# Performance work log

Measured on AMD Instinct MI355X. Metric: run time of the kernel, lower is better.

## Reference

```python
import jax, jax.numpy as jnp
import numpy as np
import math

CHUNK = 64

def _linear(x, W, b):
    # torch nn.Linear: y = x @ W.T + b
    return jnp.einsum('bsd,ed->bse', x, W) + b

def setup_inputs() -> dict:
    key = jax.random.key(0)
    ks = jax.random.split(key, 10)
    B, S, D = 4, 4096, 512
    scale = 0.02
    inp = {
        'x': jax.random.normal(ks[0], (B, S, D), jnp.float32),
        'base_phases': jax.random.normal(ks[1], (S, D), jnp.float32) * math.pi,
        'Wk': jax.random.normal(ks[2], (D, D), jnp.float32) * scale,
        'bk': jnp.zeros((D,), jnp.float32),
        'Wv': jax.random.normal(ks[3], (D, D), jnp.float32) * scale,
        'bv': jnp.zeros((D,), jnp.float32),
        'Wq': jax.random.normal(ks[4], (D, D), jnp.float32) * scale,
        'bq': jnp.zeros((D,), jnp.float32),
        'Wkm': jax.random.normal(ks[5], (D, D), jnp.float32) * scale,
        'bkm': jnp.zeros((D,), jnp.float32),
        'Wqm': jax.random.normal(ks[6], (D, D), jnp.float32) * scale,
        'bqm': jnp.zeros((D,), jnp.float32),
        'mod_scale': jnp.ones((1,), jnp.float32) * 0.1,
        'ln_g': jnp.ones((D,), jnp.float32),
        'ln_b': jnp.zeros((D,), jnp.float32),
        'Wo': jax.random.normal(ks[7], (D, D), jnp.float32) * scale,
        'bo': jnp.zeros((D,), jnp.float32),
    }
    return inp

def reference(x, base_phases, Wk, bk, Wv, bv, Wq, bq, Wkm, bkm, Wqm, bqm, mod_scale, ln_g, ln_b, Wo, bo):
    B, S, D = x.shape
    bp = base_phases[:S][None]                      # [1,S,D]
    key = _linear(x, Wk, bk)
    value = _linear(x, Wv, bv)
    query = _linear(x, Wq, bq)
    key_phase = bp + _linear(key, Wkm, bkm) * mod_scale
    query_phase = bp + _linear(query, Wqm, bqm) * mod_scale
    bound_real = value * jnp.cos(key_phase)
    bound_imag = value * jnp.sin(key_phase)
    # chunked cumulative memory (S divisible by CHUNK -> no padding)
    nC = S // CHUNK
    br = bound_real.reshape(B, nC, CHUNK, D)
    bi = bound_imag.reshape(B, nC, CHUNK, D)
    qp = query_phase.reshape(B, nC, CHUNK, D)
    mem_real = jnp.cumsum(br, axis=2)
    mem_imag = jnp.cumsum(bi, axis=2)
    retrieved = (mem_real * jnp.cos(qp) + mem_imag * jnp.sin(qp)).reshape(B, S, D)
    retrieved = retrieved / math.sqrt(D)
    # LayerNorm + Linear (to_out)
    mu = jnp.mean(retrieved, axis=-1, keepdims=True)
    var = jnp.mean((retrieved - mu) ** 2, axis=-1, keepdims=True)
    normed = (retrieved - mu) / jnp.sqrt(var + 1e-5) * ln_g + ln_b
    out = _linear(normed, Wo, bo)
    return x + out
```

## Files before the change

### kernel.cpp

```cpp
#include <hip/hip_runtime.h>
#include <hip/hip_bf16.h>


typedef __attribute__((ext_vector_type(8))) short short8;
typedef __attribute__((ext_vector_type(4))) float f32x4;

#define M_TOK   16384
#define DIM     512
#define NCHUNK  64

__device__ __forceinline__ void gll16(const void* g, void* l) {
  __builtin_amdgcn_global_load_lds(
      (const __attribute__((address_space(1))) unsigned int*)g,
      (__attribute__((address_space(3))) unsigned int*)l, 16, 0, 0);
}

__device__ __forceinline__ uint2 pack4bf(float4 v) {
  union { __hip_bfloat16 h[4]; uint2 u; } t;
  t.h[0] = __float2bfloat16(v.x);
  t.h[1] = __float2bfloat16(v.y);
  t.h[2] = __float2bfloat16(v.z);
  t.h[3] = __float2bfloat16(v.w);
  return t.u;
}

__global__ __launch_bounds__(256) void cvt_f32_bf16(
    const float* __restrict__ s, __hip_bfloat16* __restrict__ d, int n4) {
  int i = blockIdx.x * 256 + threadIdx.x;
  if (i >= n4) return;
  ((uint2*)d)[i] = pack4bf(((const float4*)s)[i]);
}

__global__ __launch_bounds__(256) void prep(
    const float* __restrict__ Wv, const float* __restrict__ Wo,
    const float* __restrict__ bv,
    const float* __restrict__ Wkm, const float* __restrict__ Wqm,
    const float* __restrict__ Wk, const float* __restrict__ Wq,
    const float* __restrict__ bk, const float* __restrict__ bkm,
    const float* __restrict__ bq, const float* __restrict__ bqm,
    __hip_bfloat16* __restrict__ Wall, float* __restrict__ bc1,
    __hip_bfloat16* __restrict__ Wm_bf, __hip_bfloat16* __restrict__ WT_bf) {
  const int b = blockIdx.x;
  const int tid = threadIdx.x;
  if (b < 512) {
    int m = b >> 8;
    int idx = ((b & 255) * 256 + tid) * 4;
    const float* src = m ? Wo : Wv;
    __hip_bfloat16* dst = Wall + (m ? (size_t)1536 * 512 : 0);
    ((uint2*)dst)[idx >> 2] = pack4bf(*(const float4*)(src + idx));
    int t = b * 256 + tid;
    if (t < 512) bc1[t] = bv[t];
  } else if (b < 1024) {
    int bb = b - 512;
    int m = bb >> 8;
    int idx = ((bb & 255) * 256 + tid) * 4;
    const float* src = m ? Wqm : Wkm;
    ((uint2*)(Wm_bf + (size_t)m * 262144))[idx >> 2] =
        pack4bf(*(const float4*)(src + idx));
  } else if (b < 1152) {
    __shared__ float tile[64][65];
    int bb = b - 1024;
    int z = bb >> 6;
    int tl = bb & 63;
    int tr = tl >> 3, tc = tl & 7;
    const float* src = z ? Wq : Wk;
#pragma unroll
    for (int i = 0; i < 4; i++) {
      int r = (tid >> 4) + 16 * i;
      int c4 = (tid & 15) * 4;
      float4 v = *(const float4*)(src + (size_t)(tr * 64 + r) * 512 +
                                  tc * 64 + c4);
      tile[r][c4 + 0] = v.x;
      tile[r][c4 + 1] = v.y;
      tile[r][c4 + 2] = v.z;
      tile[r][c4 + 3] = v.w;
    }
    __syncthreads();
    int orow = tid >> 2;
    int seg = tid & 3;
    __hip_bfloat16* dst = WT_bf + (size_t)z * 262144 +
                          (size_t)(tc * 64 + orow) * 512 + tr * 64 + seg * 16;
#pragma unroll
    for (int q = 0; q < 4; q++) {
      float4 v;
      v.x = tile[seg * 16 + q * 4 + 0][orow];
      v.y = tile[seg * 16 + q * 4 + 1][orow];
      v.z = tile[seg * 16 + q * 4 + 2][orow];
      v.w = tile[seg * 16 + q * 4 + 3][orow];
      *(uint2*)(dst + q * 4) = pack4bf(v);
    }
  } else {
    int row = (b - 1152) * 4 + (tid >> 6);
    int lane = tid & 63;
    int z = row >> 9;
    int i = row & 511;
    const float* Wm = z ? Wqm : Wkm;
    const float* b0 = z ? bq : bk;
    const float* bm = z ? bqm : bkm;
    const float4* w4 = (const float4*)(Wm + (size_t)i * 512 + lane * 8);
    const float4* v4 = (const float4*)(b0 + lane * 8);
    float4 w0 = w4[0], w1 = w4[1], c0 = v4[0], c1 = v4[1];
    float acc = w0.x * c0.x + w0.y * c0.y + w0.z * c0.z + w0.w * c0.w +
                w1.x * c1.x + w1.y * c1.y + w1.z * c1.z + w1.w * c1.w;
#pragma unroll
    for (int off = 32; off; off >>= 1) acc += __shfl_xor(acc, off, 64);
    if (lane == 0) bc1[512 + z * 512 + i] = acc + bm[i];
  }
}

template <int EPI>
__global__ __launch_bounds__(256) void gemm_bt(
    const __hip_bfloat16* __restrict__ A, int lda,
    const __hip_bfloat16* __restrict__ Bt,
    const float* __restrict__ bias,
    void* __restrict__ Cout, int ldc,
    const float* __restrict__ resid) {
  constexpr int K = 512, BK = 32;
  __shared__ __align__(16) __hip_bfloat16 As[128 * BK];
  __shared__ __align__(16) __hip_bfloat16 Bs[128 * BK];

  const int tid  = threadIdx.x;
  const int lane = tid & 63;
  const int w    = tid >> 6;
  const int wm   = w >> 1;
  const int wn   = w & 1;
  const int m0   = blockIdx.y * 128;
  const int n0   = blockIdx.x * 128;

  const int rS0    = (w * 2 + 0) * 16 + (lane >> 2);
  const int rS1    = (w * 2 + 1) * 16 + (lane >> 2);
  const int kInRow = (lane & 3) * 8;
  const __hip_bfloat16* gA0 = A + (size_t)(m0 + rS0) * lda + kInRow;
  const __hip_bfloat16* gA1 = A + (size_t)(m0 + rS1) * lda + kInRow;
  const __hip_bfloat16* gB0 = Bt + (size_t)(n0 + rS0) * K + kInRow;
  const __hip_bfloat16* gB1 = Bt + (size_t)(n0 + rS1) * K + kInRow;
  char* ldsA0 = (char*)As + (w * 2 + 0) * 1024;
  char* ldsA1 = (char*)As + (w * 2 + 1) * 1024;
  char* ldsB0 = (char*)Bs + (w * 2 + 0) * 1024;
  char* ldsB1 = (char*)Bs + (w * 2 + 1) * 1024;

  f32x4 acc[4][4] = {};

  const int rfA = lane & 15;
  const int rfK = (lane >> 4) * 8;

  for (int kt = 0; kt < K; kt += BK) {
    __syncthreads();
    gll16(gA0 + kt, ldsA0);
    gll16(gA1 + kt, ldsA1);
    gll16(gB0 + kt, ldsB0);
    gll16(gB1 + kt, ldsB1);
    __syncthreads();

    short8 af[4], bf[4];
#pragma unroll
    for (int i = 0; i < 4; i++)
      af[i] = *(const short8*)(As + (wm * 64 + i * 16 + rfA) * BK + rfK);
#pragma unroll
    for (int j = 0; j < 4; j++)
      bf[j] = *(const short8*)(Bs + (wn * 64 + j * 16 + rfA) * BK + rfK);
#pragma unroll
    for (int i = 0; i < 4; i++)
#pragma unroll
      for (int j = 0; j < 4; j++)
        acc[i][j] = __builtin_amdgcn_mfma_f32_16x16x32_bf16(
            af[i], bf[j], acc[i][j], 0, 0, 0);
  }

  const int cq = lane >> 4;
#pragma unroll
  for (int i = 0; i < 4; i++) {
    int row = m0 + wm * 64 + i * 16 + cq * 4;
#pragma unroll
    for (int j = 0; j < 4; j++) {
      int col = n0 + wn * 64 + j * 16 + (lane & 15);
      float bz = bias[col];
#pragma unroll
      for (int r = 0; r < 4; r++) {
        float v = acc[i][j][r] + bz;
        size_t o = (size_t)(row + r) * ldc + col;
        if (EPI == 0) {
          ((__hip_bfloat16*)Cout)[o] = __float2bfloat16(v);
        } else {
          ((float*)Cout)[o] = v + resid[o];
        }
      }
    }
  }
}

__global__ __launch_bounds__(256) void gemm_compose(
    const __hip_bfloat16* __restrict__ Wm_bf,
    const __hip_bfloat16* __restrict__ WT_bf,
    __hip_bfloat16* __restrict__ Wall) {
  constexpr int K = 512, BK = 32;
  const __hip_bfloat16* A  = Wm_bf + (size_t)blockIdx.z * 262144;
  const __hip_bfloat16* Bt = WT_bf + (size_t)blockIdx.z * 262144;
  __hip_bfloat16* C = Wall + (size_t)(512 + blockIdx.z * 512) * 512;
  __shared__ __align__(16) __hip_bfloat16 As[128 * BK];
  __shared__ __align__(16) __hip_bfloat16 Bs[128 * BK];

  const int tid  = threadIdx.x;
  const int lane = tid & 63;
  const int w    = tid >> 6;
  const int wm   = w >> 1;
  const int wn   = w & 1;
  const int m0   = blockIdx.y * 128;
  const int n0   = blockIdx.x * 128;

  const int rS0    = (w * 2 + 0) * 16 + (lane >> 2);
  const int rS1    = (w * 2 + 1) * 16 + (lane >> 2);
  const int kInRow = (lane & 3) * 8;
  const __hip_bfloat16* gA0 = A + (size_t)(m0 + rS0) * K + kInRow;
  const __hip_bfloat16* gA1 = A + (size_t)(m0 + rS1) * K + kInRow;
  const __hip_bfloat16* gB0 = Bt + (size_t)(n0 + rS0) * K + kInRow;
  const __hip_bfloat16* gB1 = Bt + (size_t)(n0 + rS1) * K + kInRow;
  char* ldsA0 = (char*)As + (w * 2 + 0) * 1024;
  char* ldsA1 = (char*)As + (w * 2 + 1) * 1024;
  char* ldsB0 = (char*)Bs + (w * 2 + 0) * 1024;
  char* ldsB1 = (char*)Bs + (w * 2 + 1) * 1024;

  f32x4 acc[4][4] = {};
  const int rfA = lane & 15;
  const int rfK = (lane >> 4) * 8;

  for (int kt = 0; kt < K; kt += BK) {
    __syncthreads();
    gll16(gA0 + kt, ldsA0);
    gll16(gA1 + kt, ldsA1);
    gll16(gB0 + kt, ldsB0);
    gll16(gB1 + kt, ldsB1);
    __syncthreads();

    short8 af[4], bf[4];
#pragma unroll
    for (int i = 0; i < 4; i++)
      af[i] = *(const short8*)(As + (wm * 64 + i * 16 + rfA) * BK + rfK);
#pragma unroll
    for (int j = 0; j < 4; j++)
      bf[j] = *(const short8*)(Bs + (wn * 64 + j * 16 + rfA) * BK + rfK);
#pragma unroll
    for (int i = 0; i < 4; i++)
#pragma unroll
      for (int j = 0; j < 4; j++)
        acc[i][j] = __builtin_amdgcn_mfma_f32_16x16x32_bf16(
            af[i], bf[j], acc[i][j], 0, 0, 0);
  }

  const int cq = lane >> 4;
#pragma unroll
  for (int i = 0; i < 4; i++) {
    int row = m0 + wm * 64 + i * 16 + cq * 4;
#pragma unroll
    for (int j = 0; j < 4; j++) {
      int col = n0 + wn * 64 + j * 16 + (lane & 15);
#pragma unroll
      for (int r = 0; r < 4; r++)
        C[(size_t)(row + r) * 512 + col] = __float2bfloat16(acc[i][j][r]);
    }
  }
}

__global__ __launch_bounds__(512) void phase_cumsum_ln(
    const __hip_bfloat16* __restrict__ VKQ,
    const float* __restrict__ bp,
    const float* __restrict__ mod_scale,
    const float* __restrict__ ln_g, const float* __restrict__ ln_b,
    __hip_bfloat16* __restrict__ normed) {
  __shared__ __hip_bfloat16 R[64 * 512];
  const int d      = threadIdx.x;
  const int blk    = blockIdx.x;
  const int token0 = blk * 64;
  const int sg0    = (blk & (NCHUNK - 1)) * 64;
  const float msc  = mod_scale[0];
  const float inv_sqrt_d = 0.044194173824159216f;

  float mr = 0.f, mi = 0.f;
  for (int s = 0; s < 64; ++s) {
    size_t t = (size_t)(token0 + s);
    float v  = __bfloat162float(VKQ[t * 1536 + d]);
    float km = __bfloat162float(VKQ[t * 1536 + 512 + d]);
    float qm = __bfloat162float(VKQ[t * 1536 + 1024 + d]);
    float b  = bp[(size_t)(sg0 + s) * 512 + d];
    float kp = b + km * msc;
    float qp = b + qm * msc;
    float sk, ck, sq, cq;
    __sincosf(kp, &sk, &ck);
    __sincosf(qp, &sq, &cq);
    mr += v * ck;
    mi += v * sk;
    R[s * 512 + d] = __float2bfloat16((mr * cq + mi * sq) * inv_sqrt_d);
  }
  __syncthreads();

  const int lane = threadIdx.x & 63;
  const int wv   = threadIdx.x >> 6;
  float gj[8], bj[8];
#pragma unroll
  for (int j = 0; j < 8; j++) {
    int col = lane + 64 * j;
    gj[j] = ln_g[col];
    bj[j] = ln_b[col];
  }
  for (int rr = 0; rr < 8; ++rr) {
    int row = wv * 8 + rr;
    float vals[8], sum = 0.f, sq2 = 0.f;
#pragma unroll
    for (int j = 0; j < 8; j++) {
      float x = __bfloat162float(R[row * 512 + lane + 64 * j]);
      vals[j] = x;
      sum += x;
      sq2 += x * x;
    }
#pragma unroll
    for (int off = 32; off; off >>= 1) {
      sum += __shfl_xor(sum, off, 64);
      sq2 += __shfl_xor(sq2, off, 64);
    }
    float mu   = sum * (1.f / 512.f);
    float var  = sq2 * (1.f / 512.f) - mu * mu;
    float rstd = rsqrtf(var + 1e-5f);
    size_t base = (size_t)(token0 + row) * 512;
#pragma unroll
    for (int j = 0; j < 8; j++) {
      int col = lane + 64 * j;
      float nv = (vals[j] - mu) * rstd * gj[j] + bj[j];
      normed[base + col] = __float2bfloat16(nv);
    }
  }
}

extern "C" void kernel_launch(void* const* d_in, const int* in_sizes, int n_in,
                              void* d_out, int out_size, void* d_ws,
                              size_t ws_size, hipStream_t stream) {
  const float* x    = (const float*)d_in[0];
  const float* bp   = (const float*)d_in[1];
  const float* Wk   = (const float*)d_in[2];
  const float* bk   = (const float*)d_in[3];
  const float* Wv   = (const float*)d_in[4];
  const float* bv   = (const float*)d_in[5];
  const float* Wq   = (const float*)d_in[6];
  const float* bq   = (const float*)d_in[7];
  const float* Wkm  = (const float*)d_in[8];
  const float* bkm  = (const float*)d_in[9];
  const float* Wqm  = (const float*)d_in[10];
  const float* bqm  = (const float*)d_in[11];
  const float* msc  = (const float*)d_in[12];
  const float* lng  = (const float*)d_in[13];
  const float* lnb  = (const float*)d_in[14];
  const float* Wo   = (const float*)d_in[15];
  const float* bo   = (const float*)d_in[16];
  float* out = (float*)d_out;

  char* ws = (char*)d_ws;
  __hip_bfloat16* x_bf  = (__hip_bfloat16*)ws;  ws += (size_t)M_TOK * DIM * 2;
  __hip_bfloat16* Wall  = (__hip_bfloat16*)ws;  ws += (size_t)2048 * 512 * 2;
  __hip_bfloat16* Wm_bf = (__hip_bfloat16*)ws;  ws += (size_t)2 * 262144 * 2;
  __hip_bfloat16* WT_bf = (__hip_bfloat16*)ws;  ws += (size_t)2 * 262144 * 2;
  float*          bc1   = (float*)ws;           ws += 1536 * 4;
  __hip_bfloat16* VKQ   = (__hip_bfloat16*)ws;  ws += (size_t)M_TOK * 1536 * 2;
  __hip_bfloat16* nrm   = (__hip_bfloat16*)ws;  ws += (size_t)M_TOK * DIM * 2;

  cvt_f32_bf16<<<8192, 256, 0, stream>>>(x, x_bf, 2097152);
  prep<<<1408, 256, 0, stream>>>(Wv, Wo, bv, Wkm, Wqm, Wk, Wq, bk, bkm, bq,
                                 bqm, Wall, bc1, Wm_bf, WT_bf);
  gemm_compose<<<dim3(4, 4, 2), 256, 0, stream>>>(Wm_bf, WT_bf, Wall);
  gemm_bt<0><<<dim3(12, 128), 256, 0, stream>>>(x_bf, DIM, Wall, bc1, VKQ,
                                                1536, nullptr);
  phase_cumsum_ln<<<256, 512, 0, stream>>>(VKQ, bp, msc, lng, lnb, nrm);
  gemm_bt<1><<<dim3(4, 128), 256, 0, stream>>>(nrm, DIM,
                                               Wall + (size_t)1536 * 512, bo,
                                               out, DIM, x);
}
```

Before: 211.9 us.

## Fuse output GEMM into phase/cumsum/LayerNorm kernel and interleave VKQ layout

Merges the x conversion into the weight prep kernel, stores the V/K/Q projection output interleaved per feature (stride 4) so each thread reads v, km and qm with one 8-byte load, and fuses the final Wo GEMM plus bias and residual into the cumsum/LayerNorm kernel using the LDS-resident normalized tile. This removes the normed intermediate round trip and two launches. The fused output GEMM reads Wo straight from global without LDS staging, and only 256 blocks do the output matmul, so MFMA utilization and parallelism there may be lower. The interleaved layout also pads the buffer to 2048 columns per row.

Result: slower. 245.7 us (+16.0%).

```diff
diff --git a/kernel.cpp b/kernel.cpp
--- a/kernel.cpp
+++ b/kernel.cpp
@@ -8,6 +8,7 @@
 #define M_TOK   16384
 #define DIM     512
 #define NCHUNK  64
+#define RPAD    520
 
 __device__ __forceinline__ void gll16(const void* g, void* l) {
   __builtin_amdgcn_global_load_lds(
@@ -24,14 +25,8 @@
   return t.u;
 }
 
-__global__ __launch_bounds__(256) void cvt_f32_bf16(
-    const float* __restrict__ s, __hip_bfloat16* __restrict__ d, int n4) {
-  int i = blockIdx.x * 256 + threadIdx.x;
-  if (i >= n4) return;
-  ((uint2*)d)[i] = pack4bf(((const float4*)s)[i]);
-}
-
-__global__ __launch_bounds__(256) void prep(
+__global__ __launch_bounds__(256) void prep_all(
+    const float* __restrict__ x, __hip_bfloat16* __restrict__ x_bf,
     const float* __restrict__ Wv, const float* __restrict__ Wo,
     const float* __restrict__ bv,
     const float* __restrict__ Wkm, const float* __restrict__ Wqm,
@@ -40,8 +35,13 @@
     const float* __restrict__ bq, const float* __restrict__ bqm,
     __hip_bfloat16* __restrict__ Wall, float* __restrict__ bc1,
     __hip_bfloat16* __restrict__ Wm_bf, __hip_bfloat16* __restrict__ WT_bf) {
-  const int b = blockIdx.x;
   const int tid = threadIdx.x;
+  if (blockIdx.x < 8192) {
+    int i = blockIdx.x * 256 + tid;
+    ((uint2*)x_bf)[i] = pack4bf(((const float4*)x)[i]);
+    return;
+  }
+  const int b = blockIdx.x - 8192;
   if (b < 512) {
     int m = b >> 8;
     int idx = ((b & 255) * 256 + tid) * 4;
@@ -113,8 +113,7 @@
     const __hip_bfloat16* __restrict__ A, int lda,
     const __hip_bfloat16* __restrict__ Bt,
     const float* __restrict__ bias,
-    void* __restrict__ Cout, int ldc,
-    const float* __restrict__ resid) {
+    void* __restrict__ Cout, int ldc) {
   constexpr int K = 512, BK = 32;
   __shared__ __align__(16) __hip_bfloat16 As[128 * BK];
   __shared__ __align__(16) __hip_bfloat16 Bs[128 * BK];
@@ -178,11 +177,12 @@
 #pragma unroll
       for (int r = 0; r < 4; r++) {
         float v = acc[i][j][r] + bz;
-        size_t o = (size_t)(row + r) * ldc + col;
         if (EPI == 0) {
+          ((__hip_bfloat16*)Cout)[(size_t)(row + r) * ldc + col] =
+              __float2bfloat16(v);
+        } else {
+          size_t o = (size_t)(row + r) * 2048 + (col & 511) * 4 + (col >> 9);
           ((__hip_bfloat16*)Cout)[o] = __float2bfloat16(v);
-        } else {
-          ((float*)Cout)[o] = v + resid[o];
         }
       }
     }
@@ -261,71 +261,126 @@
   }
 }
 
-__global__ __launch_bounds__(512) void phase_cumsum_ln(
+__global__ __launch_bounds__(512) void fused_pg(
     const __hip_bfloat16* __restrict__ VKQ,
     const float* __restrict__ bp,
     const float* __restrict__ mod_scale,
     const float* __restrict__ ln_g, const float* __restrict__ ln_b,
-    __hip_bfloat16* __restrict__ normed) {
-  __shared__ __hip_bfloat16 R[64 * 512];
-  const int d      = threadIdx.x;
+    const __hip_bfloat16* __restrict__ WoB,
+    const float* __restrict__ bo,
+    const float* __restrict__ x,
+    float* __restrict__ out) {
+  __shared__ __hip_bfloat16 R[64 * RPAD];
+  const int tid    = threadIdx.x;
   const int blk    = blockIdx.x;
   const int token0 = blk * 64;
   const int sg0    = (blk & (NCHUNK - 1)) * 64;
   const float msc  = mod_scale[0];
   const float inv_sqrt_d = 0.044194173824159216f;
 
-  float mr = 0.f, mi = 0.f;
-  for (int s = 0; s < 64; ++s) {
-    size_t t = (size_t)(token0 + s);
-    float v  = __bfloat162float(VKQ[t * 1536 + d]);
-    float km = __bfloat162float(VKQ[t * 1536 + 512 + d]);
-    float qm = __bfloat162float(VKQ[t * 1536 + 1024 + d]);
-    float b  = bp[(size_t)(sg0 + s) * 512 + d];
-    float kp = b + km * msc;
-    float qp = b + qm * msc;
-    float sk, ck, sq, cq;
-    __sincosf(kp, &sk, &ck);
-    __sincosf(qp, &sq, &cq);
-    mr += v * ck;
-    mi += v * sk;
-    R[s * 512 + d] = __float2bfloat16((mr * cq + mi * sq) * inv_sqrt_d);
+  {
+    const int d = tid;
+    float mr = 0.f, mi = 0.f;
+    const __hip_bfloat16* vb = VKQ + (size_t)token0 * 2048 + d * 4;
+    const float* bb = bp + (size_t)sg0 * 512 + d;
+#pragma unroll 4
+    for (int s = 0; s < 64; ++s) {
+      union { uint2 u; __hip_bfloat16 h[4]; } p;
+      p.u = *(const uint2*)(vb + (size_t)s * 2048);
+      float b  = bb[(size_t)s * 512];
+      float v  = __bfloat162float(p.h[0]);
+      float km = __bfloat162float(p.h[1]);
+      float qm = __bfloat162float(p.h[2]);
+      float kp = b + km * msc;
+      float qp = b + qm * msc;
+      float sk, ck, sq, cq;
+      __sincosf(kp, &sk, &ck);
+      __sincosf(qp, &sq, &cq);
+      mr += v * ck;
+      mi += v * sk;
+      R[s * RPAD + d] = __float2bfloat16((mr * cq + mi * sq) * inv_sqrt_d);
+    }
   }
   __syncthreads();
 
-  const int lane = threadIdx.x & 63;
-  const int wv   = threadIdx.x >> 6;
-  float gj[8], bj[8];
-#pragma unroll
-  for (int j = 0; j < 8; j++) {
-    int col = lane + 64 * j;
-    gj[j] = ln_g[col];
-    bj[j] = ln_b[col];
-  }
-  for (int rr = 0; rr < 8; ++rr) {
-    int row = wv * 8 + rr;
-    float vals[8], sum = 0.f, sq2 = 0.f;
-#pragma unroll
-    for (int j = 0; j < 8; j++) {
-      float x = __bfloat162float(R[row * 512 + lane + 64 * j]);
-      vals[j] = x;
-      sum += x;
-      sq2 += x * x;
-    }
-#pragma unroll
-    for (int off = 32; off; off >>= 1) {
-      sum += __shfl_xor(sum, off, 64);
-      sq2 += __shfl_xor(sq2, off, 64);
-    }
-    float mu   = sum * (1.f / 512.f);
-    float var  = sq2 * (1.f / 512.f) - mu * mu;
-    float rstd = rsqrtf(var + 1e-5f);
-    size_t base = (size_t)(token0 + row) * 512;
+  {
+    const int lane = tid & 63;
+    const int wv   = tid >> 6;
+    float gj[8], bj[8];
 #pragma unroll
     for (int j = 0; j < 8; j++) {
       int col = lane + 64 * j;
-      float nv = (vals[j] - mu) * rstd * gj[j] + bj[j];
-      normed[base + col] = __float2bfloat16(nv);
+      gj[j] = ln_g[col];
+      bj[j] = ln_b[col];
+    }
+    for (int rr = 0; rr < 8; ++rr) {
+      int row = wv * 8 + rr;
+      float vals[8], sum = 0.f, sq2 = 0.f;
+#pragma unroll
+      for (int j = 0; j < 8; j++) {
+        float v = __bfloat162float(R[row * RPAD + lane + 64 * j]);
+        vals[j] = v;
+        sum += v;
+        sq2 += v * v;
+      }
+#pragma unroll
+      for (int off = 32; off; off >>= 1) {
+        sum += __shfl_xor(sum, off, 64);
+        sq2 += __shfl_xor(sq2, off, 64);
+      }
+      float mu   = sum * (1.f / 512.f);
+      float var  = sq2 * (1.f / 512.f) - mu * mu;
+      float rstd = rsqrtf(var + 1e-5f);
+#pragma unroll
+      for (int j = 0; j < 8; j++) {
+        float nv = (vals[j] - mu) * rstd * gj[j] + bj[j];
+        R[row * RPAD + lane + 64 * j] = __float2bfloat16(nv);
+      }
+    }
+  }
+  __syncthreads();
+
+  {
+    const int lane = tid & 63;
+    const int w    = tid >> 6;
+    const int rfA  = lane & 15;
+    const int rfK  = (lane >> 4) * 8;
+    f32x4 acc[4][4] = {};
+
+    for (int kt = 0; kt < 512; kt += 32) {
+      short8 af[4], bf[4];
+#pragma unroll
+      for (int j = 0; j < 4; j++) {
+        int col = w * 64 + j * 16 + rfA;
+        bf[j] = *(const short8*)(WoB + (size_t)col * 512 + kt + rfK);
+      }
+#pragma unroll
+      for (int i = 0; i < 4; i++)
+        af[i] = *(const short8*)(R + (i * 16 + rfA) * RPAD + kt + rfK);
+#pragma unroll
+      for (int i = 0; i < 4; i++)
+#pragma unroll
+        for (int j = 0; j < 4; j++)
+          acc[i][j] = __builtin_amdgcn_mfma_f32_16x16x32_bf16(
+              af[i], bf[j], acc[i][j], 0, 0, 0);
+    }
+
+    const int cq = lane >> 4;
+    float bz[4];
+#pragma unroll
+    for (int j = 0; j < 4; j++) bz[j] = bo[w * 64 + j * 16 + (lane & 15)];
+#pragma unroll
+    for (int i = 0; i < 4; i++) {
+      int row = token0 + i * 16 + cq * 4;
+#pragma unroll
+      for (int j = 0; j < 4; j++) {
+        int col = w * 64 + j * 16 + (lane & 15);
+#pragma unroll
+        for (int r = 0; r < 4; r++) {
+          size_t o = (size_t)(row + r) * 512 + col;
+          out[o] = acc[i][j][r] + bz[j] + x[o];
+        }
+      }
     }
   }
 }
@@ -358,17 +413,14 @@
   __hip_bfloat16* Wm_bf = (__hip_bfloat16*)ws;  ws += (size_t)2 * 262144 * 2;
   __hip_bfloat16* WT_bf = (__hip_bfloat16*)ws;  ws += (size_t)2 * 262144 * 2;
   float*          bc1   = (float*)ws;           ws += 1536 * 4;
-  __hip_bfloat16* VKQ   = (__hip_bfloat16*)ws;  ws += (size_t)M_TOK * 1536 * 2;
-  __hip_bfloat16* nrm   = (__hip_bfloat16*)ws;  ws += (size_t)M_TOK * DIM * 2;
-
-  cvt_f32_bf16<<<8192, 256, 0, stream>>>(x, x_bf, 2097152);
-  prep<<<1408, 256, 0, stream>>>(Wv, Wo, bv, Wkm, Wqm, Wk, Wq, bk, bkm, bq,
-                                 bqm, Wall, bc1, Wm_bf, WT_bf);
+  __hip_bfloat16* VKQ   = (__hip_bfloat16*)ws;  ws += (size_t)M_TOK * 2048 * 2;
+
+  prep_all<<<9600, 256, 0, stream>>>(x, x_bf, Wv, Wo, bv, Wkm, Wqm, Wk, Wq,
+                                     bk, bkm, bq, bqm, Wall, bc1, Wm_bf,
+                                     WT_bf);
   gemm_compose<<<dim3(4, 4, 2), 256, 0, stream>>>(Wm_bf, WT_bf, Wall);
-  gemm_bt<0><<<dim3(12, 128), 256, 0, stream>>>(x_bf, DIM, Wall, bc1, VKQ,
-                                                1536, nullptr);
-  phase_cumsum_ln<<<256, 512, 0, stream>>>(VKQ, bp, msc, lng, lnb, nrm);
-  gemm_bt<1><<<dim3(4, 128), 256, 0, stream>>>(nrm, DIM,
-                                               Wall + (size_t)1536 * 512, bo,
-                                               out, DIM, x);
-}
+  gemm_bt<2><<<dim3(12, 128), 256, 0, stream>>>(x_bf, DIM, Wall, bc1, VKQ,
+                                                2048);
+  fused_pg<<<256, 512, 0, stream>>>(VKQ, bp, msc, lng, lnb,
+                                    Wall + (size_t)1536 * 512, bo, x, out);
+}
```
